# Optimization experiments

Measured on AMD Instinct MI355X. Metric: run time of the kernel, lower is better.

The kernel has to match this reference:

```python
import jax, jax.numpy as jnp
import numpy as np

B, S, E, H, MLP = 2, 2048, 1024, 16, 4096
VEC = 8          # args.vec_length: block-row height of vector-sparse mask
SPARSITY = 0.9   # fraction of attention entries dropped
D = E // H


def _make_mask():
    # static_random_mask_aligned: each block-row of VEC query rows keeps a
    # random ~(1-sparsity) subset of key columns. Diagonal kept so every
    # softmax row is non-empty.
    rng = np.random.default_rng(0)
    block = rng.random((S // VEC, S)) < (1.0 - SPARSITY)   # [m, n]
    mask = np.repeat(block, VEC, axis=0)                   # [S, S]
    mask |= np.eye(S, dtype=bool)
    return jnp.asarray(mask)


def setup_inputs() -> dict:
    key = jax.random.key(0)
    ks = jax.random.split(key, 8)
    w = lambda k, shp: (0.02 * jax.random.normal(k, shp, dtype=jnp.float32))
    return {
        "x": jax.random.normal(ks[0], (B, S, E), dtype=jnp.float32),
        "mask": _make_mask(),                       # [S,S] bool, static
        "w_qkv": w(ks[1], (3 * E, E)),             # in_proj_weight
        "b_qkv": jnp.zeros((3 * E,), jnp.float32),
        "w_out": w(ks[2], (E, E)),                 # out_proj
        "b_out": jnp.zeros((E,), jnp.float32),
        "g1": jnp.ones((E,), jnp.float32), "beta1": jnp.zeros((E,), jnp.float32),
        "g2": jnp.ones((E,), jnp.float32), "beta2": jnp.zeros((E,), jnp.float32),
        "w1": w(ks[3], (MLP, E)), "bias1": jnp.zeros((MLP,), jnp.float32),
        "w2": w(ks[4], (E, MLP)), "bias2": jnp.zeros((E,), jnp.float32),
    }


def _layer_norm(x, g, b, eps=1e-5):
    mu = jnp.mean(x, axis=-1, keepdims=True)
    var = jnp.mean(jnp.square(x - mu), axis=-1, keepdims=True)
    return (x - mu) * jax.lax.rsqrt(var + eps) * g + b


def _sparse_mha(h, mask, w_qkv, b_qkv, w_out, b_out):
    qkv = jnp.einsum("bse,fe->bsf", h, w_qkv) + b_qkv       # [B,S,3E]
    q, k, v = jnp.split(qkv, 3, axis=-1)
    q = q.reshape(B, S, H, D)
    k = k.reshape(B, S, H, D)
    v = v.reshape(B, S, H, D)
    scores = jnp.einsum("bqhd,bkhd->bhqk", q, k) / jnp.sqrt(jnp.float32(D))
    scores = jnp.where(mask[None, None], scores, jnp.float32(-1e9))
    p = jax.nn.softmax(scores, axis=-1)
    ctx = jnp.einsum("bhqk,bkhd->bqhd", p, v).reshape(B, S, E)
    return jnp.einsum("bse,fe->bsf", ctx, w_out) + b_out


def reference(x, mask, w_qkv, b_qkv, w_out, b_out, g1, beta1, g2, beta2,
              w1, bias1, w2, bias2):
    h = _layer_norm(x, g1, beta1)
    attn = _sparse_mha(h, mask, w_qkv, b_qkv, w_out, b_out)
    out = attn + x                      # residual 1
    out = _layer_norm(out, g2, beta2)
    out = jnp.einsum("bse,me->bsm", out, w1) + bias1   # linear1 (no activation, as in source)
    out = jnp.einsum("bsm,em->bse", out, w2) + bias2   # linear2
    return out + x                      # residual adds ORIGINAL x (as in source)
```

## Files before the change

### kernel.cpp

```cpp
#include <hip/hip_runtime.h>
#include <cstdint>
#include <cstddef>

typedef unsigned short u16;
typedef unsigned int u32;
typedef short s16x8 __attribute__((ext_vector_type(8)));
typedef float f32x4 __attribute__((ext_vector_type(4)));
typedef _Float16 f16x2 __attribute__((ext_vector_type(2)));

__device__ __forceinline__ float fdot2(f16x2 a, f16x2 b, float c) {
#if defined(__HIP_DEVICE_COMPILE__) && __has_builtin(__builtin_amdgcn_fdot2)
  return __builtin_amdgcn_fdot2(a, b, c, false);
#else
  return (float)a.x * (float)b.x + (float)a.y * (float)b.y + c;
#endif
}

__device__ __forceinline__ float red8(float x) {
#if defined(__HIP_DEVICE_COMPILE__) && __has_builtin(__builtin_amdgcn_update_dpp)
  int xi = __float_as_int(x);
  x += __int_as_float(__builtin_amdgcn_update_dpp(0, xi, 0xB1, 0xF, 0xF, true));
  xi = __float_as_int(x);
  x += __int_as_float(__builtin_amdgcn_update_dpp(0, xi, 0x4E, 0xF, 0xF, true));
  xi = __float_as_int(x);
  x += __int_as_float(__builtin_amdgcn_update_dpp(0, xi, 0x141, 0xF, 0xF, true));
  return x;
#else
  x += __shfl_xor(x, 1); x += __shfl_xor(x, 2); x += __shfl_xor(x, 4);
  return x;
#endif
}

#define S_LEN 2048
#define EMB   1024
#define NHEAD 16
#define HD    64
#define E3    3072
#define MLPD  4096
#define NROWS 4096
#define LCAP  640

__device__ __forceinline__ float bf2f(u16 v) {
  union { u32 i; float f; } c; c.i = ((u32)v) << 16; return c.f;
}
__device__ __forceinline__ u16 f2bf(float f) {
  union { float f; u32 i; } c; c.f = f;
  u32 x = c.i;
  return (u16)((x + 0x7FFFu + ((x >> 16) & 1u)) >> 16);
}
__device__ __forceinline__ u16 f2h(float f) {
  _Float16 h = (_Float16)f;
  union { _Float16 h; u16 b; } c; c.h = h; return c.b;
}

__device__ __forceinline__ void gl2lds16(const void* g, void* l) {
  __builtin_amdgcn_global_load_lds(
      (__attribute__((address_space(1))) void*)(g),
      (__attribute__((address_space(3))) void*)(l), 16, 0, 0);
}

__global__ void detect_flags(const u32* __restrict__ w1s, int* __restrict__ dtflag,
                             const u32* __restrict__ mask, int* __restrict__ maskrep) {
  __shared__ int hits[256];
  __shared__ u32 red[256];
  int h = 0; u32 v = 0;
  for (int i = threadIdx.x; i < 4096; i += 256) {
    u32 w = w1s[i];
    if ((w & 0xFFFFu) && (((w >> 7) & 0xFFu) >= 0xC8u)) ++h;
    v |= mask[i];
  }
  hits[threadIdx.x] = h; red[threadIdx.x] = v;
  __syncthreads();
  if (threadIdx.x == 0) {
    int t = 0; u32 o = 0;
    for (int i = 0; i < 256; ++i) { t += hits[i]; o |= red[i]; }
    *dtflag = (t > 8) ? 1 : 0;
    int rep;
    if (o <= 1u) rep = 0;
    else if (o & 0x80u) rep = 1;
    else if (o & 0x00800000u) rep = 2;
    else rep = 3;
    *maskrep = rep;
  }
}

__device__ __forceinline__ bool maskbit(const void* m, int rep, size_t idx) {
  switch (rep) {
    case 0:  return ((const int*)m)[idx] != 0;
    case 1:  return ((const u16*)m)[idx] != 0;
    case 2:  return ((const u32*)m)[idx] != 0;
    default: return ((const unsigned char*)m)[idx] != 0;
  }
}

__global__ __launch_bounds__(256)
void cvt_kernel(const void* __restrict__ src, u16* __restrict__ dst,
                int n8, const int* __restrict__ dtflag) {
  const int i = blockIdx.x * blockDim.x + threadIdx.x;
  if (i >= n8) return;
  if (*dtflag) {
    const float4 a = ((const float4*)src)[i * 2];
    const float4 b = ((const float4*)src)[i * 2 + 1];
    u16 o[8] = {f2bf(a.x), f2bf(a.y), f2bf(a.z), f2bf(a.w),
                f2bf(b.x), f2bf(b.y), f2bf(b.z), f2bf(b.w)};
    *(uint4*)(dst + (size_t)i * 8) = *(const uint4*)o;
  } else {
    ((uint4*)dst)[i] = ((const uint4*)src)[i];
  }
}

__global__ void cvt_small(const void* s0, u16* d0, const void* s1, u16* d1,
                          const void* s2, u16* d2, const void* s3, u16* d3,
                          const void* s4, u16* d4, const void* s5, u16* d5,
                          const void* s6, u16* d6, const void* s7, u16* d7,
                          const int* __restrict__ dtflag) {
  const int f = *dtflag;
  const void* srcs[8] = {s0, s1, s2, s3, s4, s5, s6, s7};
  u16* dsts[8] = {d0, d1, d2, d3, d4, d5, d6, d7};
  const int ns[8] = {E3, EMB, EMB, EMB, EMB, EMB, MLPD, EMB};
#pragma unroll
  for (int k = 0; k < 8; ++k) {
    for (int idx = threadIdx.x; idx < ns[k]; idx += 256)
      dsts[k][idx] = f ? f2bf(((const float*)srcs[k])[idx])
                       : ((const u16*)srcs[k])[idx];
  }
}

__global__ void build_lists(const void* __restrict__ mask, const int* __restrict__ repf,
                            int* __restrict__ lists, int* __restrict__ cnt,
                            unsigned char* __restrict__ diagflag) {
  __shared__ int num;
  const int m = blockIdx.x;
  if (threadIdx.x == 0) num = 0;
  __syncthreads();
  const int rep = *repf;
  const int row0 = m * 8;
  for (int j = threadIdx.x; j < S_LEN; j += 256) {
    int srcrow = (j == row0) ? (row0 + 1) : row0;
    bool bit = maskbit(mask, rep, (size_t)srcrow * S_LEN + j);
    if (j >= row0 && j < row0 + 8) diagflag[j] = bit ? 0 : 1;
    if (bit) {
      int p = atomicAdd(&num, 1);
      if (p < LCAP) lists[m * LCAP + p] = j * 2048;
    }
  }
  __syncthreads();
  if (threadIdx.x == 0) cnt[m] = (num < LCAP) ? num : LCAP;
}

__global__ __launch_bounds__(256)
void ln_kernel(const void* __restrict__ Xv, const u16* __restrict__ g,
               const u16* __restrict__ be, u16* __restrict__ O,
               const int* __restrict__ inf32) {
  const int wv = threadIdx.x >> 6, ln = threadIdx.x & 63;
  const int row = blockIdx.x * 4 + wv;
  float v[16];
  if (inf32 && *inf32) {
    const float* xr = (const float*)Xv + (size_t)row * EMB;
    float4 a0 = *(const float4*)(xr + ln * 8);
    float4 a1 = *(const float4*)(xr + ln * 8 + 4);
    float4 b0 = *(const float4*)(xr + 512 + ln * 8);
    float4 b1 = *(const float4*)(xr + 512 + ln * 8 + 4);
    v[0]=a0.x; v[1]=a0.y; v[2]=a0.z; v[3]=a0.w; v[4]=a1.x; v[5]=a1.y; v[6]=a1.z; v[7]=a1.w;
    v[8]=b0.x; v[9]=b0.y; v[10]=b0.z; v[11]=b0.w; v[12]=b1.x; v[13]=b1.y; v[14]=b1.z; v[15]=b1.w;
  } else {
    const u16* xr = (const u16*)Xv + (size_t)row * EMB;
    union { uint4 u; u16 s[8]; } p0, p1;
    p0.u = *(const uint4*)(xr + ln * 8);
    p1.u = *(const uint4*)(xr + 512 + ln * 8);
#pragma unroll
    for (int t = 0; t < 8; ++t) { v[t] = bf2f(p0.s[t]); v[8 + t] = bf2f(p1.s[t]); }
  }
  float s = 0.f, sq = 0.f;
#pragma unroll
  for (int t = 0; t < 16; ++t) { s += v[t]; sq += v[t] * v[t]; }
#pragma unroll
  for (int off = 32; off; off >>= 1) { s += __shfl_xor(s, off); sq += __shfl_xor(sq, off); }
  const float mu = s * (1.0f / EMB);
  const float var = sq * (1.0f / EMB) - mu * mu;
  const float rsig = rsqrtf(var + 1e-5f);
  union { uint4 u; u16 s[8]; } g0, g1v, b0, b1v, o0, o1;
  g0.u = *(const uint4*)(g + ln * 8);   g1v.u = *(const uint4*)(g + 512 + ln * 8);
  b0.u = *(const uint4*)(be + ln * 8);  b1v.u = *(const uint4*)(be + 512 + ln * 8);
#pragma unroll
  for (int t = 0; t < 8; ++t) {
    o0.s[t] = f2bf((v[t]     - mu) * rsig * bf2f(g0.s[t])  + bf2f(b0.s[t]));
    o1.s[t] = f2bf((v[8 + t] - mu) * rsig * bf2f(g1v.s[t]) + bf2f(b1v.s[t]));
  }
  u16* orow = O + (size_t)row * EMB;
  *(uint4*)(orow + ln * 8) = o0.u;
  *(uint4*)(orow + 512 + ln * 8) = o1.u;
}

__global__ __launch_bounds__(256)
void gemm_bt(const u16* __restrict__ A, const u16* __restrict__ B,
             const u16* __restrict__ bias, u16* __restrict__ C,
             int M, int N, int K) {
  __shared__ u16 a_sh[128 * 64];
  __shared__ u16 b_sh[128 * 64];
  const int tid = threadIdx.x;
  const int wv = tid >> 6, ln = tid & 63;
  const int wm = wv & 1, wn = wv >> 1;
  const int tm = blockIdx.y, tn = blockIdx.x;
  const int srow = ln >> 3;
  const int scol = ((ln & 7) ^ srow) * 8;
  const int q = ln >> 4, rr = ln & 15;

  f32x4 acc[4][4] = {};
  const u16* Abase = A + (size_t)(tm * 128) * K;
  const u16* Bbase = B + (size_t)(tn * 128) * K;

  for (int k0 = 0; k0 < K; k0 += 64) {
    __syncthreads();
#pragma unroll
    for (int c = 0; c < 4; ++c) {
      const int chunk = wv * 4 + c;
      const int row = chunk * 8 + srow;
      gl2lds16(Abase + (size_t)row * K + k0 + scol, &a_sh[chunk * 512]);
      gl2lds16(Bbase + (size_t)row * K + k0 + scol, &b_sh[chunk * 512]);
    }
    __syncthreads();
#pragma unroll
    for (int kk = 0; kk < 2; ++kk) {
      const int slot = ((kk * 4 + q) ^ (rr & 7)) * 8;
      s16x8 af[4], bfr[4];
#pragma unroll
      for (int mi = 0; mi < 4; ++mi)
        af[mi] = *(const s16x8*)&a_sh[(wm * 64 + mi * 16 + rr) * 64 + slot];
#pragma unroll
      for (int ni = 0; ni < 4; ++ni)
        bfr[ni] = *(const s16x8*)&b_sh[(wn * 64 + ni * 16 + rr) * 64 + slot];
#pragma unroll
      for (int mi = 0; mi < 4; ++mi)
#pragma unroll
        for (int ni = 0; ni < 4; ++ni)
          acc[mi][ni] = __builtin_amdgcn_mfma_f32_16x16x32_bf16(af[mi], bfr[ni], acc[mi][ni], 0, 0, 0);
    }
  }
#pragma unroll
  for (int ni = 0; ni < 4; ++ni) {
    const int col = tn * 128 + wn * 64 + ni * 16 + rr;
    const float bv = bf2f(bias[col]);
#pragma unroll
    for (int mi = 0; mi < 4; ++mi)
#pragma unroll
      for (int r2 = 0; r2 < 4; ++r2) {
        const int row = tm * 128 + wm * 64 + mi * 16 + q * 4 + r2;
        C[(size_t)row * N + col] = f2bf(acc[mi][ni][r2] + bv);
      }
  }
}

__global__ __launch_bounds__(256)
void gemm_bt_sk(const u16* __restrict__ A, const u16* __restrict__ B,
                u16* __restrict__ P0, u16* __restrict__ P1,
                int M, int N, int K) {
  __shared__ u16 a_sh[128 * 64];
  __shared__ u16 b_sh[128 * 64];
  const int tid = threadIdx.x;
  const int wv = tid >> 6, ln = tid & 63;
  const int wm = wv & 1, wn = wv >> 1;
  const int tm = blockIdx.y, tn = blockIdx.x, kz = blockIdx.z;
  const int Kh = K >> 1;
  const int koff = kz * Kh;
  const int srow = ln >> 3;
  const int scol = ((ln & 7) ^ srow) * 8;
  const int q = ln >> 4, rr = ln & 15;

  f32x4 acc[4][4] = {};
  const u16* Abase = A + (size_t)(tm * 128) * K + koff;
  const u16* Bbase = B + (size_t)(tn * 128) * K + koff;

  for (int k0 = 0; k0 < Kh; k0 += 64) {
    __syncthreads();
#pragma unroll
    for (int c = 0; c < 4; ++c) {
      const int chunk = wv * 4 + c;
      const int row = chunk * 8 + srow;
      gl2lds16(Abase + (size_t)row * K + k0 + scol, &a_sh[chunk * 512]);
      gl2lds16(Bbase + (size_t)row * K + k0 + scol, &b_sh[chunk * 512]);
    }
    __syncthreads();
#pragma unroll
    for (int kk = 0; kk < 2; ++kk) {
      const int slot = ((kk * 4 + q) ^ (rr & 7)) * 8;
      s16x8 af[4], bfr[4];
#pragma unroll
      for (int mi = 0; mi < 4; ++mi)
        af[mi] = *(const s16x8*)&a_sh[(wm * 64 + mi * 16 + rr) * 64 + slot];
#pragma unroll
      for (int ni = 0; ni < 4; ++ni)
        bfr[ni] = *(const s16x8*)&b_sh[(wn * 64 + ni * 16 + rr) * 64 + slot];
#pragma unroll
      for (int mi = 0; mi < 4; ++mi)
#pragma unroll
        for (int ni = 0; ni < 4; ++ni)
          acc[mi][ni] = __builtin_amdgcn_mfma_f32_16x16x32_bf16(af[mi], bfr[ni], acc[mi][ni], 0, 0, 0);
    }
  }
  u16* P = kz ? P1 : P0;
#pragma unroll
  for (int ni = 0; ni < 4; ++ni) {
    const int col = tn * 128 + wn * 64 + ni * 16 + rr;
#pragma unroll
    for (int mi = 0; mi < 4; ++mi)
#pragma unroll
      for (int r2 = 0; r2 < 4; ++r2) {
        const int row = tm * 128 + wm * 64 + mi * 16 + q * 4 + r2;
        P[(size_t)row * N + col] = f2bf(acc[mi][ni][r2]);
      }
  }
}

__global__ __launch_bounds__(256)
void combine_kernel(const u16* __restrict__ P0, const u16* __restrict__ P1,
                    const u16* __restrict__ bias, const void* __restrict__ xr,
                    void* __restrict__ Ov, const int* __restrict__ f32io) {
  const int i = blockIdx.x * 256 + threadIdx.x;
  const int col8 = (i & 127) * 8;
  union { uint4 u; u16 s[8]; } a, b, bi;
  a.u = ((const uint4*)P0)[i];
  b.u = ((const uint4*)P1)[i];
  bi.u = *(const uint4*)(bias + col8);
  const int f = *f32io;
  float o[8];
#pragma unroll
  for (int t = 0; t < 8; ++t) o[t] = bf2f(a.s[t]) + bf2f(b.s[t]) + bf2f(bi.s[t]);
  if (f) {
    const float4 x0 = ((const float4*)xr)[i * 2];
    const float4 x1 = ((const float4*)xr)[i * 2 + 1];
    o[0]+=x0.x; o[1]+=x0.y; o[2]+=x0.z; o[3]+=x0.w;
    o[4]+=x1.x; o[5]+=x1.y; o[6]+=x1.z; o[7]+=x1.w;
    float4 r0 = {o[0],o[1],o[2],o[3]}, r1 = {o[4],o[5],o[6],o[7]};
    ((float4*)Ov)[i * 2] = r0;
    ((float4*)Ov)[i * 2 + 1] = r1;
  } else {
    union { uint4 u; u16 s[8]; } xv;
    xv.u = ((const uint4*)xr)[i];
    u16 r[8];
#pragma unroll
    for (int t = 0; t < 8; ++t) r[t] = f2bf(o[t] + bf2f(xv.s[t]));
    ((uint4*)Ov)[i] = *(const uint4*)r;
  }
}

__global__ __launch_bounds__(256)
void gemm_qkv(const u16* __restrict__ A, const u16* __restrict__ B,
              const u16* __restrict__ bias,
              u16* __restrict__ Qb, u16* __restrict__ Kp, u16* __restrict__ Vp,
              int K) {
  __shared__ u16 a_sh[128 * 64];
  __shared__ u16 b_sh[128 * 64];
  const int tid = threadIdx.x;
  const int wv = tid >> 6, ln = tid & 63;
  const int wm = wv & 1, wn = wv >> 1;
  const int tm = blockIdx.y, tn = blockIdx.x;
  const int srow = ln >> 3;
  const int scol = ((ln & 7) ^ srow) * 8;
  const int q = ln >> 4, rr = ln & 15;

  f32x4 acc[4][4] = {};
  const u16* Abase = A + (size_t)(tm * 128) * K;
  const u16* Bbase = B + (size_t)(tn * 128) * K;

  for (int k0 = 0; k0 < K; k0 += 64) {
    __syncthreads();
#pragma unroll
    for (int c = 0; c < 4; ++c) {
      const int chunk = wv * 4 + c;
      const int row = chunk * 8 + srow;
      gl2lds16(Abase + (size_t)row * K + k0 + scol, &a_sh[chunk * 512]);
      gl2lds16(Bbase + (size_t)row * K + k0 + scol, &b_sh[chunk * 512]);
    }
    __syncthreads();
#pragma unroll
    for (int kk = 0; kk < 2; ++kk) {
      const int slot = ((kk * 4 + q) ^ (rr & 7)) * 8;
      s16x8 af[4], bfr[4];
#pragma unroll
      for (int mi = 0; mi < 4; ++mi)
        af[mi] = *(const s16x8*)&a_sh[(wm * 64 + mi * 16 + rr) * 64 + slot];
#pragma unroll
      for (int ni = 0; ni < 4; ++ni)
        bfr[ni] = *(const s16x8*)&b_sh[(wn * 64 + ni * 16 + rr) * 64 + slot];
#pragma unroll
      for (int mi = 0; mi < 4; ++mi)
#pragma unroll
        for (int ni = 0; ni < 4; ++ni)
          acc[mi][ni] = __builtin_amdgcn_mfma_f32_16x16x32_bf16(af[mi], bfr[ni], acc[mi][ni], 0, 0, 0);
    }
  }
  const int third = (tn * 128) >> 10;
#pragma unroll
  for (int ni = 0; ni < 4; ++ni) {
    const int col = tn * 128 + wn * 64 + ni * 16 + rr;
    const int w = col & 1023;
    const float bv = bf2f(bias[col]);
#pragma unroll
    for (int mi = 0; mi < 4; ++mi)
#pragma unroll
      for (int r2 = 0; r2 < 4; ++r2) {
        const int row = tm * 128 + wm * 64 + mi * 16 + q * 4 + r2;
        const float o = acc[mi][ni][r2] + bv;
        const size_t idx = (size_t)row * 1024 + w;
        if (third == 0)      Qb[idx] = f2bf(o);
        else if (third == 1) Kp[idx] = f2h(o);
        else                 Vp[idx] = f2h(o);
      }
  }
}

__global__ __launch_bounds__(256)
void gemm_bt_n64(const u16* __restrict__ A, const u16* __restrict__ B,
                 const u16* __restrict__ bias, const void* __restrict__ resid,
                 void* __restrict__ Cv, int M, int N, int K,
                 const int* __restrict__ residf32, const int* __restrict__ outf32) {
  __shared__ u16 a_sh[128 * 64];
  __shared__ u16 b_sh[64 * 64];
  const int tid = threadIdx.x;
  const int wv = tid >> 6, ln = tid & 63;
  const int wm = wv & 1, wn = wv >> 1;
  const int tm = blockIdx.y, tn = blockIdx.x;
  const int srow = ln >> 3;
  const int scol = ((ln & 7) ^ srow) * 8;
  const int q = ln >> 4, rr = ln & 15;

  f32x4 acc[4][2] = {};
  const u16* Abase = A + (size_t)(tm * 128) * K;
  const u16* Bbase = B + (size_t)(tn * 64) * K;

  for (int k0 = 0; k0 < K; k0 += 64) {
    __syncthreads();
#pragma unroll
    for (int c = 0; c < 4; ++c) {
      const int chunk = wv * 4 + c;
      const int row = chunk * 8 + srow;
      gl2lds16(Abase + (size_t)row * K + k0 + scol, &a_sh[chunk * 512]);
    }
#pragma unroll
    for (int c = 0; c < 2; ++c) {
      const int chunk = wv * 2 + c;
      const int row = chunk * 8 + srow;
      gl2lds16(Bbase + (size_t)row * K + k0 + scol, &b_sh[chunk * 512]);
    }
    __syncthreads();
#pragma unroll
    for (int kk = 0; kk < 2; ++kk) {
      const int slot = ((kk * 4 + q) ^ (rr & 7)) * 8;
      s16x8 af[4], bfr[2];
#pragma unroll
      for (int mi = 0; mi < 4; ++mi)
        af[mi] = *(const s16x8*)&a_sh[(wm * 64 + mi * 16 + rr) * 64 + slot];
#pragma unroll
      for (int ni = 0; ni < 2; ++ni)
        bfr[ni] = *(const s16x8*)&b_sh[(wn * 32 + ni * 16 + rr) * 64 + slot];
#pragma unroll
      for (int mi = 0; mi < 4; ++mi)
#pragma unroll
        for (int ni = 0; ni < 2; ++ni)
          acc[mi][ni] = __builtin_amdgcn_mfma_f32_16x16x32_bf16(af[mi], bfr[ni], acc[mi][ni], 0, 0, 0);
    }
  }
  const int rf32 = residf32 ? *residf32 : 0;
  const int f32o = outf32 ? *outf32 : 0;
#pragma unroll
  for (int ni = 0; ni < 2; ++ni) {
    const int col = tn * 64 + wn * 32 + ni * 16 + rr;
    const float bv = bf2f(bias[col]);
#pragma unroll
    for (int mi = 0; mi < 4; ++mi)
#pragma unroll
      for (int r2 = 0; r2 < 4; ++r2) {
        const int row = tm * 128 + wm * 64 + mi * 16 + q * 4 + r2;
        const size_t idx = (size_t)row * N + col;
        float o = acc[mi][ni][r2] + bv;
        if (resid)
          o += rf32 ? ((const float*)resid)[idx] : bf2f(((const u16*)resid)[idx]);
        if (f32o) ((float*)Cv)[idx] = o;
        else      ((u16*)Cv)[idx] = f2bf(o);
      }
  }
}

__global__ __launch_bounds__(512)
void attn_kernel(const u16* __restrict__ Qb, const u16* __restrict__ Kp,
                 const u16* __restrict__ Vp, const int* __restrict__ lists,
                 const int* __restrict__ cnt, const unsigned char* __restrict__ diagflag,
                 u16* __restrict__ ctx) {
  __shared__ int list_sh[LCAP];
  const int g = blockIdx.x;
  const int b = g >> 12;
  const int h = (g >> 8) & 15;
  const int m = g & 255;
  const int tid = threadIdx.x, wv = tid >> 6, ln = tid & 63;
  const int es = ln >> 3, dc = ln & 7;
  const int i = m * 8 + wv;
  const int n = cnt[m];

  for (int e = tid; e < n; e += 512) list_sh[e] = lists[m * LCAP + e];
  __syncthreads();

  const u16* qrow = Qb + (size_t)(b * S_LEN + i) * EMB + h * 64 + dc * 8;
  union { uint4 u; u16 s[8]; } qi; qi.u = *(const uint4*)qrow;
  f16x2 q2[4];
#pragma unroll
  for (int t = 0; t < 4; ++t) {
    q2[t].x = (_Float16)(bf2f(qi.s[2 * t])     * 0.125f);
    q2[t].y = (_Float16)(bf2f(qi.s[2 * t + 1]) * 0.125f);
  }

  const char* kbase = (const char*)Kp + (size_t)b * S_LEN * 2048 + h * 128 + dc * 16;
  const char* vbase = (const char*)Vp + (size_t)b * S_LEN * 2048 + h * 128 + dc * 16;

  float sum = 0.f;
  float acc[8] = {};

  auto score = [&](const uint4& ku) -> float {
    union { uint4 u; f16x2 p[4]; } kk; kk.u = ku;
    float s = fdot2(kk.p[3], q2[3], fdot2(kk.p[2], q2[2],
              fdot2(kk.p[1], q2[1], fdot2(kk.p[0], q2[0], 0.f))));
    s = red8(s);
    return __expf(fminf(fmaxf(s, -60.f), 60.f));
  };
  auto doV = [&](const uint4& vu, float p) {
    union { uint4 u; _Float16 hh[8]; } vv; vv.u = vu;
#pragma unroll
    for (int t = 0; t < 8; ++t) acc[t] += (float)vv.hh[t] * p;
  };

  const int df = diagflag[i];
  if (df) {
    const int dioff = i * 2048;
    const uint4 ku = *(const uint4*)(kbase + dioff);
    const uint4 vu = *(const uint4*)(vbase + dioff);
    float p = score(ku);
    p = (es == 0) ? p : 0.f;
    sum += p;
    doV(vu, p);
  }

  int e0 = 0;
  for (; e0 + 32 <= n; e0 += 32) {
    const int oA = list_sh[e0 + es];
    const int oB = list_sh[e0 + 8 + es];
    const int oC = list_sh[e0 + 16 + es];
    const int oD = list_sh[e0 + 24 + es];
    const uint4 kA = *(const uint4*)(kbase + (size_t)oA);
    const uint4 kB = *(const uint4*)(kbase + (size_t)oB);
    const uint4 kC = *(const uint4*)(kbase + (size_t)oC);
    const uint4 kD = *(const uint4*)(kbase + (size_t)oD);
    const uint4 vA = *(const uint4*)(vbase + (size_t)oA);
    const uint4 vB = *(const uint4*)(vbase + (size_t)oB);
    const uint4 vC = *(const uint4*)(vbase + (size_t)oC);
    const uint4 vD = *(const uint4*)(vbase + (size_t)oD);
    const float pA = score(kA);
    const float pB = score(kB);
    const float pC = score(kC);
    const float pD = score(kD);
    sum += (pA + pB) + (pC + pD);
    doV(vA, pA);
    doV(vB, pB);
    doV(vC, pC);
    doV(vD, pD);
  }
  for (; e0 + 8 <= n; e0 += 8) {
    const int off = list_sh[e0 + es];
    const uint4 ku = *(const uint4*)(kbase + (size_t)off);
    const uint4 vu = *(const uint4*)(vbase + (size_t)off);
    const float p = score(ku);
    sum += p;
    doV(vu, p);
  }
  if (e0 < n) {
    const int e = e0 + es;
    const bool valid = (e < n);
    const int off = valid ? list_sh[e] : list_sh[0];
    const uint4 ku = *(const uint4*)(kbase + (size_t)off);
    const uint4 vu = *(const uint4*)(vbase + (size_t)off);
    float p = score(ku);
    p = valid ? p : 0.f;
    sum += p;
    doV(vu, p);
  }

#pragma unroll
  for (int off = 8; off < 64; off <<= 1) {
    sum += __shfl_xor(sum, off);
#pragma unroll
    for (int t = 0; t < 8; ++t) acc[t] += __shfl_xor(acc[t], off);
  }

  if (es == 0) {
    const float inv = 1.0f / sum;
    u16 o[8];
#pragma unroll
    for (int t = 0; t < 8; ++t) o[t] = f2bf(acc[t] * inv);
    *(uint4*)(ctx + (size_t)(b * S_LEN + i) * EMB + h * 64 + dc * 8) = *(const uint4*)o;
  }
}

extern "C" void kernel_launch(void* const* d_in, const int* in_sizes, int n_in,
                              void* d_out, int out_size, void* d_ws, size_t ws_size,
                              hipStream_t stream) {
  const void* x_raw    = d_in[0];
  const void* mask     = d_in[1];
  const void* wqkv_raw = d_in[2];
  const void* bqkv_raw = d_in[3];
  const void* wout_raw = d_in[4];
  const void* bout_raw = d_in[5];
  const void* g1_raw   = d_in[6];
  const void* be1_raw  = d_in[7];
  const void* g2_raw   = d_in[8];
  const void* be2_raw  = d_in[9];
  const void* w1_raw   = d_in[10];
  const void* b1_raw   = d_in[11];
  const void* w2_raw   = d_in[12];
  const void* b2_raw   = d_in[13];

  char* ws = (char*)d_ws;
  const size_t MB = 1u << 20;
  int* dtflag         = (int*)ws;
  int* maskrep        = (int*)(ws + 64);
  int* cnt            = (int*)(ws + 1024);
  unsigned char* dfl  = (unsigned char*)(ws + 4096);
  int* lists          = (int*)(ws + 8192);
  u16* R1  = (u16*)(ws + 1 * MB);
  u16* Qb  = (u16*)(ws + 9 * MB);
  u16* Kp  = (u16*)(ws + 17 * MB);
  u16* Vp  = (u16*)(ws + 25 * MB);
  u16* M1  = (u16*)(ws + 17 * MB);
  u16* W   = (u16*)(ws + 49 * MB);
  char* sm = ws + 57 * MB;
  u16* bq  = (u16*)(sm);
  u16* bo  = (u16*)(sm + 8192);
  u16* g1b = (u16*)(sm + 16384);
  u16* be1b= (u16*)(sm + 24576);
  u16* g2b = (u16*)(sm + 32768);
  u16* be2b= (u16*)(sm + 40960);
  u16* b1b = (u16*)(sm + 49152);
  u16* b2b = (u16*)(sm + 65536);

  detect_flags<<<dim3(1), dim3(256), 0, stream>>>((const u32*)w1_raw, dtflag,
                                                  (const u32*)mask, maskrep);
  build_lists<<<dim3(256), dim3(256), 0, stream>>>(mask, maskrep, lists, cnt, dfl);
  cvt_small<<<dim3(1), dim3(256), 0, stream>>>(
      bqkv_raw, bq, bout_raw, bo, g1_raw, g1b, be1_raw, be1b,
      g2_raw, g2b, be2_raw, be2b, b1_raw, b1b, b2_raw, b2b, dtflag);

  auto cvt = [&](const void* src, u16* dst, int n) {
    const int n8 = n / 8;
    cvt_kernel<<<dim3((n8 + 255) / 256), dim3(256), 0, stream>>>(src, dst, n8, dtflag);
  };

  ln_kernel<<<dim3(NROWS / 4), dim3(256), 0, stream>>>(x_raw, g1b, be1b, R1, dtflag);
  cvt(wqkv_raw, W, E3 * EMB);
  gemm_qkv<<<dim3(E3 / 128, NROWS / 128), dim3(256), 0, stream>>>(
      R1, W, bq, Qb, Kp, Vp, EMB);
  attn_kernel<<<dim3(2 * NHEAD * 256), dim3(512), 0, stream>>>(
      Qb, Kp, Vp, lists, cnt, dfl, R1);
  cvt(wout_raw, W, EMB * EMB);
  gemm_bt_n64<<<dim3(EMB / 64, NROWS / 128), dim3(256), 0, stream>>>(
      R1, W, bo, x_raw, Qb, NROWS, EMB, EMB, dtflag, nullptr);
  ln_kernel<<<dim3(NROWS / 4), dim3(256), 0, stream>>>(Qb, g2b, be2b, R1, nullptr);
  cvt(w1_raw, W, MLPD * EMB);
  gemm_bt<<<dim3(MLPD / 128, NROWS / 128), dim3(256), 0, stream>>>(
      R1, W, b1b, M1, NROWS, MLPD, EMB);
  cvt(w2_raw, W, EMB * MLPD);
  gemm_bt_sk<<<dim3(EMB / 128, NROWS / 128, 2), dim3(256), 0, stream>>>(
      M1, W, R1, Qb, NROWS, EMB, MLPD);
  combine_kernel<<<dim3(NROWS * EMB / 8 / 256), dim3(256), 0, stream>>>(
      R1, Qb, b2b, x_raw, d_out, dtflag);
}
```

Measured before the change: 456.9 us.

## Interleave K and V per head and use fma_mix/exp2 in sparse attention

The QKV GEMM now writes K and V into one interleaved buffer where each head's K and V rows sit side by side, so each gathered key's K and V loads hit adjacent 128-byte segments, with 32-bit offsets instead of size_t. The attention inner loop folds log2(e) into the query scale and uses exp2f, replaces the fp16-to-fp32 convert-and-FMA in the V accumulation with v_fma_mix_f32 inline asm, and writes the DPP reduction as inline v_add_f32_dpp. These aim to cut memory transactions and VALU instructions in the gather-bound attention loop. The exp clamp range changes and inline asm brings portability and correctness risk.

```diff
diff --git a/kernel.cpp b/kernel.cpp
--- a/kernel.cpp
+++ b/kernel.cpp
@@ -17,17 +17,34 @@
 }
 
 __device__ __forceinline__ float red8(float x) {
-#if defined(__HIP_DEVICE_COMPILE__) && __has_builtin(__builtin_amdgcn_update_dpp)
-  int xi = __float_as_int(x);
-  x += __int_as_float(__builtin_amdgcn_update_dpp(0, xi, 0xB1, 0xF, 0xF, true));
-  xi = __float_as_int(x);
-  x += __int_as_float(__builtin_amdgcn_update_dpp(0, xi, 0x4E, 0xF, 0xF, true));
-  xi = __float_as_int(x);
-  x += __int_as_float(__builtin_amdgcn_update_dpp(0, xi, 0x141, 0xF, 0xF, true));
+#if defined(__HIP_DEVICE_COMPILE__)
+  asm("v_add_f32_dpp %0, %0, %0 quad_perm:[1,0,3,2] row_mask:0xf bank_mask:0xf"
+      : "+v"(x));
+  asm("v_add_f32_dpp %0, %0, %0 quad_perm:[2,3,0,1] row_mask:0xf bank_mask:0xf"
+      : "+v"(x));
+  asm("v_add_f32_dpp %0, %0, %0 row_half_mirror row_mask:0xf bank_mask:0xf"
+      : "+v"(x));
   return x;
 #else
   x += __shfl_xor(x, 1); x += __shfl_xor(x, 2); x += __shfl_xor(x, 4);
   return x;
+#endif
+}
+
+__device__ __forceinline__ void fmamix_lo(float& a, u32 hv, float p) {
+#if defined(__HIP_DEVICE_COMPILE__)
+  asm("v_fma_mix_f32 %0, %1, %2, %0 op_sel_hi:[1,0,0]"
+      : "+v"(a) : "v"(hv), "v"(p));
+#else
+  union { u32 i; _Float16 h[2]; } c; c.i = hv; a += (float)c.h[0] * p;
+#endif
+}
+__device__ __forceinline__ void fmamix_hi(float& a, u32 hv, float p) {
+#if defined(__HIP_DEVICE_COMPILE__)
+  asm("v_fma_mix_f32 %0, %1, %2, %0 op_sel:[1,0,0] op_sel_hi:[1,0,0]"
+      : "+v"(a) : "v"(hv), "v"(p));
+#else
+  union { u32 i; _Float16 h[2]; } c; c.i = hv; a += (float)c.h[1] * p;
 #endif
 }
 
@@ -141,7 +158,7 @@
     if (j >= row0 && j < row0 + 8) diagflag[j] = bit ? 0 : 1;
     if (bit) {
       int p = atomicAdd(&num, 1);
-      if (p < LCAP) lists[m * LCAP + p] = j * 2048;
+      if (p < LCAP) lists[m * LCAP + p] = j * 4096;
     }
   }
   __syncthreads();
@@ -347,7 +364,7 @@
 __global__ __launch_bounds__(256)
 void gemm_qkv(const u16* __restrict__ A, const u16* __restrict__ B,
               const u16* __restrict__ bias,
-              u16* __restrict__ Qb, u16* __restrict__ Kp, u16* __restrict__ Vp,
+              u16* __restrict__ Qb, u16* __restrict__ KVp,
               int K) {
   __shared__ u16 a_sh[128 * 64];
   __shared__ u16 b_sh[128 * 64];
@@ -402,10 +419,12 @@
       for (int r2 = 0; r2 < 4; ++r2) {
         const int row = tm * 128 + wm * 64 + mi * 16 + q * 4 + r2;
         const float o = acc[mi][ni][r2] + bv;
-        const size_t idx = (size_t)row * 1024 + w;
-        if (third == 0)      Qb[idx] = f2bf(o);
-        else if (third == 1) Kp[idx] = f2h(o);
-        else                 Vp[idx] = f2h(o);
+        if (third == 0) {
+          Qb[(size_t)row * 1024 + w] = f2bf(o);
+        } else {
+          const int hh = w >> 6, d = w & 63;
+          KVp[(size_t)row * 2048 + hh * 128 + ((third == 1) ? 0 : 64) + d] = f2h(o);
+        }
       }
   }
 }
@@ -483,8 +502,8 @@
 }
 
 __global__ __launch_bounds__(512)
-void attn_kernel(const u16* __restrict__ Qb, const u16* __restrict__ Kp,
-                 const u16* __restrict__ Vp, const int* __restrict__ lists,
+void attn_kernel(const u16* __restrict__ Qb, const u16* __restrict__ KVp,
+                 const int* __restrict__ lists,
                  const int* __restrict__ cnt, const unsigned char* __restrict__ diagflag,
                  u16* __restrict__ ctx) {
   __shared__ int list_sh[LCAP];
@@ -503,14 +522,15 @@
   const u16* qrow = Qb + (size_t)(b * S_LEN + i) * EMB + h * 64 + dc * 8;
   union { uint4 u; u16 s[8]; } qi; qi.u = *(const uint4*)qrow;
   f16x2 q2[4];
+  const float qs = 0.125f * 1.44269504f;
 #pragma unroll
   for (int t = 0; t < 4; ++t) {
-    q2[t].x = (_Float16)(bf2f(qi.s[2 * t])     * 0.125f);
-    q2[t].y = (_Float16)(bf2f(qi.s[2 * t + 1]) * 0.125f);
-  }
-
-  const char* kbase = (const char*)Kp + (size_t)b * S_LEN * 2048 + h * 128 + dc * 16;
-  const char* vbase = (const char*)Vp + (size_t)b * S_LEN * 2048 + h * 128 + dc * 16;
+    q2[t].x = (_Float16)(bf2f(qi.s[2 * t])     * qs);
+    q2[t].y = (_Float16)(bf2f(qi.s[2 * t + 1]) * qs);
+  }
+
+  const char* kvb = (const char*)KVp + (size_t)b * S_LEN * 4096;
+  const u32 loff = (u32)(h * 256 + dc * 16);
 
   float sum = 0.f;
   float acc[8] = {};
@@ -520,19 +540,21 @@
     float s = fdot2(kk.p[3], q2[3], fdot2(kk.p[2], q2[2],
               fdot2(kk.p[1], q2[1], fdot2(kk.p[0], q2[0], 0.f))));
     s = red8(s);
-    return __expf(fminf(fmaxf(s, -60.f), 60.f));
+    s = fminf(fmaxf(s, -126.f), 126.f);
+    return exp2f(s);
   };
   auto doV = [&](const uint4& vu, float p) {
-    union { uint4 u; _Float16 hh[8]; } vv; vv.u = vu;
-#pragma unroll
-    for (int t = 0; t < 8; ++t) acc[t] += (float)vv.hh[t] * p;
+    fmamix_lo(acc[0], vu.x, p); fmamix_hi(acc[1], vu.x, p);
+    fmamix_lo(acc[2], vu.y, p); fmamix_hi(acc[3], vu.y, p);
+    fmamix_lo(acc[4], vu.z, p); fmamix_hi(acc[5], vu.z, p);
+    fmamix_lo(acc[6], vu.w, p); fmamix_hi(acc[7], vu.w, p);
   };
 
   const int df = diagflag[i];
   if (df) {
-    const int dioff = i * 2048;
-    const uint4 ku = *(const uint4*)(kbase + dioff);
-    const uint4 vu = *(const uint4*)(vbase + dioff);
+    const u32 dioff = (u32)(i * 4096) + loff;
+    const uint4 ku = *(const uint4*)(kvb + dioff);
+    const uint4 vu = *(const uint4*)(kvb + dioff + 128);
     float p = score(ku);
     p = (es == 0) ? p : 0.f;
     sum += p;
@@ -541,18 +563,18 @@
 
   int e0 = 0;
   for (; e0 + 32 <= n; e0 += 32) {
-    const int oA = list_sh[e0 + es];
-    const int oB = list_sh[e0 + 8 + es];
-    const int oC = list_sh[e0 + 16 + es];
-    const int oD = list_sh[e0 + 24 + es];
-    const uint4 kA = *(const uint4*)(kbase + (size_t)oA);
-    const uint4 kB = *(const uint4*)(kbase + (size_t)oB);
-    const uint4 kC = *(const uint4*)(kbase + (size_t)oC);
-    const uint4 kD = *(const uint4*)(kbase + (size_t)oD);
-    const uint4 vA = *(const uint4*)(vbase + (size_t)oA);
-    const uint4 vB = *(const uint4*)(vbase + (size_t)oB);
-    const uint4 vC = *(const uint4*)(vbase + (size_t)oC);
-    const uint4 vD = *(const uint4*)(vbase + (size_t)oD);
+    const u32 oA = (u32)list_sh[e0 + es] + loff;
+    const u32 oB = (u32)list_sh[e0 + 8 + es] + loff;
+    const u32 oC = (u32)list_sh[e0 + 16 + es] + loff;
+    const u32 oD = (u32)list_sh[e0 + 24 + es] + loff;
+    const uint4 kA = *(const uint4*)(kvb + oA);
+    const uint4 kB = *(const uint4*)(kvb + oB);
+    const uint4 kC = *(const uint4*)(kvb + oC);
+    const uint4 kD = *(const uint4*)(kvb + oD);
+    const uint4 vA = *(const uint4*)(kvb + oA + 128);
+    const uint4 vB = *(const uint4*)(kvb + oB + 128);
+    const uint4 vC = *(const uint4*)(kvb + oC + 128);
+    const uint4 vD = *(const uint4*)(kvb + oD + 128);
     const float pA = score(kA);
     const float pB = score(kB);
     const float pC = score(kC);
@@ -564,9 +586,9 @@
     doV(vD, pD);
   }
   for (; e0 + 8 <= n; e0 += 8) {
-    const int off = list_sh[e0 + es];
-    const uint4 ku = *(const uint4*)(kbase + (size_t)off);
-    const uint4 vu = *(const uint4*)(vbase + (size_t)off);
+    const u32 off = (u32)list_sh[e0 + es] + loff;
+    const uint4 ku = *(const uint4*)(kvb + off);
+    const uint4 vu = *(const uint4*)(kvb + off + 128);
     const float p = score(ku);
     sum += p;
     doV(vu, p);
@@ -574,9 +596,9 @@
   if (e0 < n) {
     const int e = e0 + es;
     const bool valid = (e < n);
-    const int off = valid ? list_sh[e] : list_sh[0];
-    const uint4 ku = *(const uint4*)(kbase + (size_t)off);
-    const uint4 vu = *(const uint4*)(vbase + (size_t)off);
+    const u32 off = (u32)(valid ? list_sh[e] : list_sh[0]) + loff;
+    const uint4 ku = *(const uint4*)(kvb + off);
+    const uint4 vu = *(const uint4*)(kvb + off + 128);
     float p = score(ku);
     p = valid ? p : 0.f;
     sum += p;
@@ -626,8 +648,7 @@
   int* lists          = (int*)(ws + 8192);
   u16* R1  = (u16*)(ws + 1 * MB);
   u16* Qb  = (u16*)(ws + 9 * MB);
-  u16* Kp  = (u16*)(ws + 17 * MB);
-  u16* Vp  = (u16*)(ws + 25 * MB);
+  u16* KVp = (u16*)(ws + 17 * MB);
   u16* M1  = (u16*)(ws + 17 * MB);
   u16* W   = (u16*)(ws + 49 * MB);
   char* sm = ws + 57 * MB;
@@ -655,9 +676,9 @@
   ln_kernel<<<dim3(NROWS / 4), dim3(256), 0, stream>>>(x_raw, g1b, be1b, R1, dtflag);
   cvt(wqkv_raw, W, E3 * EMB);
   gemm_qkv<<<dim3(E3 / 128, NROWS / 128), dim3(256), 0, stream>>>(
-      R1, W, bq, Qb, Kp, Vp, EMB);
+      R1, W, bq, Qb, KVp, EMB);
   attn_kernel<<<dim3(2 * NHEAD * 256), dim3(512), 0, stream>>>(
-      Qb, Kp, Vp, lists, cnt, dfl, R1);
+      Qb, KVp, lists, cnt, dfl, R1);
   cvt(wout_raw, W, EMB * EMB);
   gemm_bt_n64<<<dim3(EMB / 64, NROWS / 128), dim3(256), 0, stream>>>(
       R1, W, bo, x_raw, Qb, NROWS, EMB, EMB, dtflag, nullptr);
```

Measured after the change: 469.2 us. 2.7% more time.

## Rewrite sparse attention with MFMA over interleaved per-head KV layout

Applied to the files above, without the earlier changes.

Attention is restructured so that each wave handles one 8-row query block and computes QK^T and PV with f16 MFMA instructions over 16-key chunks, replacing the scalar fdot2/DPP-reduction path. The QKV GEMM epilogue now writes K and V interleaved per (batch, head) in 256-byte rows, and pre-scales Q by 1/sqrt(d)*log2(e) in fp16 so exp2 can be used. The aim is to move score and context math onto matrix cores and to fetch K and V from one contiguous row. In exchange it adds an LDS transpose of V per chunk and fp16 probabilities, and it drops the max-subtraction in favour of a clamp.

```diff
diff --git a/kernel.cpp b/kernel.cpp
--- a/kernel.cpp
+++ b/kernel.cpp
@@ -4,32 +4,11 @@
 
 typedef unsigned short u16;
 typedef unsigned int u32;
+typedef unsigned long long u64;
 typedef short s16x8 __attribute__((ext_vector_type(8)));
 typedef float f32x4 __attribute__((ext_vector_type(4)));
-typedef _Float16 f16x2 __attribute__((ext_vector_type(2)));
-
-__device__ __forceinline__ float fdot2(f16x2 a, f16x2 b, float c) {
-#if defined(__HIP_DEVICE_COMPILE__) && __has_builtin(__builtin_amdgcn_fdot2)
-  return __builtin_amdgcn_fdot2(a, b, c, false);
-#else
-  return (float)a.x * (float)b.x + (float)a.y * (float)b.y + c;
-#endif
-}
-
-__device__ __forceinline__ float red8(float x) {
-#if defined(__HIP_DEVICE_COMPILE__) && __has_builtin(__builtin_amdgcn_update_dpp)
-  int xi = __float_as_int(x);
-  x += __int_as_float(__builtin_amdgcn_update_dpp(0, xi, 0xB1, 0xF, 0xF, true));
-  xi = __float_as_int(x);
-  x += __int_as_float(__builtin_amdgcn_update_dpp(0, xi, 0x4E, 0xF, 0xF, true));
-  xi = __float_as_int(x);
-  x += __int_as_float(__builtin_amdgcn_update_dpp(0, xi, 0x141, 0xF, 0xF, true));
-  return x;
-#else
-  x += __shfl_xor(x, 1); x += __shfl_xor(x, 2); x += __shfl_xor(x, 4);
-  return x;
-#endif
-}
+typedef _Float16 f16x4 __attribute__((ext_vector_type(4)));
+typedef _Float16 f16x8 __attribute__((ext_vector_type(8)));
 
 #define S_LEN 2048
 #define EMB   1024
@@ -141,7 +120,7 @@
     if (j >= row0 && j < row0 + 8) diagflag[j] = bit ? 0 : 1;
     if (bit) {
       int p = atomicAdd(&num, 1);
-      if (p < LCAP) lists[m * LCAP + p] = j * 2048;
+      if (p < LCAP) lists[m * LCAP + p] = j * 256;
     }
   }
   __syncthreads();
@@ -347,7 +326,7 @@
 __global__ __launch_bounds__(256)
 void gemm_qkv(const u16* __restrict__ A, const u16* __restrict__ B,
               const u16* __restrict__ bias,
-              u16* __restrict__ Qb, u16* __restrict__ Kp, u16* __restrict__ Vp,
+              u16* __restrict__ Qb, u16* __restrict__ KVp,
               int K) {
   __shared__ u16 a_sh[128 * 64];
   __shared__ u16 b_sh[128 * 64];
@@ -391,6 +370,7 @@
     }
   }
   const int third = (tn * 128) >> 10;
+  const float QS = 0.125f * 1.44269504f;
 #pragma unroll
   for (int ni = 0; ni < 4; ++ni) {
     const int col = tn * 128 + wn * 64 + ni * 16 + rr;
@@ -402,10 +382,14 @@
       for (int r2 = 0; r2 < 4; ++r2) {
         const int row = tm * 128 + wm * 64 + mi * 16 + q * 4 + r2;
         const float o = acc[mi][ni][r2] + bv;
-        const size_t idx = (size_t)row * 1024 + w;
-        if (third == 0)      Qb[idx] = f2bf(o);
-        else if (third == 1) Kp[idx] = f2h(o);
-        else                 Vp[idx] = f2h(o);
+        if (third == 0) {
+          Qb[(size_t)row * 1024 + w] = f2h(o * QS);
+        } else {
+          const int hh = w >> 6, d = w & 63;
+          const int bq_ = row >> 11, s = row & 2047;
+          KVp[((size_t)(bq_ * NHEAD + hh) * S_LEN + s) * 128 +
+              ((third == 1) ? 0 : 64) + d] = f2h(o);
+        }
       }
   }
 }
@@ -482,120 +466,122 @@
   }
 }
 
-__global__ __launch_bounds__(512)
-void attn_kernel(const u16* __restrict__ Qb, const u16* __restrict__ Kp,
-                 const u16* __restrict__ Vp, const int* __restrict__ lists,
+__global__ __launch_bounds__(256)
+void attn_kernel(const u16* __restrict__ Qb, const u16* __restrict__ KVp,
+                 const int* __restrict__ lists,
                  const int* __restrict__ cnt, const unsigned char* __restrict__ diagflag,
                  u16* __restrict__ ctx) {
-  __shared__ int list_sh[LCAP];
+  __shared__ int list_sh[4][LCAP];
+  __shared__ uint4 vsh4[4][128];
   const int g = blockIdx.x;
-  const int b = g >> 12;
-  const int h = (g >> 8) & 15;
-  const int m = g & 255;
+  const int bh = g & 31;
+  const int mq = g >> 5;
+  const int b = bh >> 4, h = bh & 15;
   const int tid = threadIdx.x, wv = tid >> 6, ln = tid & 63;
-  const int es = ln >> 3, dc = ln & 7;
-  const int i = m * 8 + wv;
+  const int lg = ln >> 4;
+  const int dl = ln & 15;
+  const int m = mq * 4 + wv;
+  const int i0 = m * 8;
+
+#pragma unroll
+  for (int w = 0; w < 4; ++w) {
+    const int nw = cnt[mq * 4 + w];
+    for (int e = tid; e < nw; e += 256) list_sh[w][e] = lists[(mq * 4 + w) * LCAP + e];
+  }
+  __syncthreads();
+
   const int n = cnt[m];
-
-  for (int e = tid; e < n; e += 512) list_sh[e] = lists[m * LCAP + e];
-  __syncthreads();
-
-  const u16* qrow = Qb + (size_t)(b * S_LEN + i) * EMB + h * 64 + dc * 8;
-  union { uint4 u; u16 s[8]; } qi; qi.u = *(const uint4*)qrow;
-  f16x2 q2[4];
-#pragma unroll
-  for (int t = 0; t < 4; ++t) {
-    q2[t].x = (_Float16)(bf2f(qi.s[2 * t])     * 0.125f);
-    q2[t].y = (_Float16)(bf2f(qi.s[2 * t + 1]) * 0.125f);
-  }
-
-  const char* kbase = (const char*)Kp + (size_t)b * S_LEN * 2048 + h * 128 + dc * 16;
-  const char* vbase = (const char*)Vp + (size_t)b * S_LEN * 2048 + h * 128 + dc * 16;
-
-  float sum = 0.f;
-  float acc[8] = {};
-
-  auto score = [&](const uint4& ku) -> float {
-    union { uint4 u; f16x2 p[4]; } kk; kk.u = ku;
-    float s = fdot2(kk.p[3], q2[3], fdot2(kk.p[2], q2[2],
-              fdot2(kk.p[1], q2[1], fdot2(kk.p[0], q2[0], 0.f))));
-    s = red8(s);
-    return __expf(fminf(fmaxf(s, -60.f), 60.f));
+  const u64 du = *(const u64*)(diagflag + i0);
+
+  f16x8 qb0 = {}, qb1 = {};
+  if (dl < 8) {
+    const u16* qr = Qb + (size_t)(b * S_LEN + i0 + dl) * EMB + h * 64 + lg * 8;
+    union { uint4 u; f16x8 h; } a0, a1;
+    a0.u = *(const uint4*)qr;
+    a1.u = *(const uint4*)(qr + 32);
+    qb0 = a0.h; qb1 = a1.h;
+  }
+
+  const char* kvb = (const char*)KVp + (size_t)bh * S_LEN * 256;
+
+  uint4* vwp = &vsh4[wv][0];
+  const int widx = ((lg >> 1) << 5) + ((dl & 3) << 3) + ((dl >> 2) << 1) + (lg & 1);
+  const u16* vrp = (const u16*)vwp + (lg << 4) + dl;
+
+  float rs = 0.f;
+  f32x4 acc[4] = {};
+
+  auto CHUNK = [&](int c0, int mode) {
+    int le;
+    if (mode == 2) {
+      le = (i0 + (dl & 7)) * 256;
+    } else {
+      const int e = c0 + dl;
+      const int idx = (mode == 1 && e >= n) ? 0 : e;
+      le = list_sh[wv][idx];
+    }
+    const char* base = kvb + le + (lg << 4);
+    union { uint4 u; f16x8 h; } ka0, ka1;
+    ka0.u = *(const uint4*)(base);
+    ka1.u = *(const uint4*)(base + 64);
+    const uint4 v0 = *(const uint4*)(base + 128);
+    const uint4 v1 = *(const uint4*)(base + 192);
+
+    f32x4 st = {};
+    st = __builtin_amdgcn_mfma_f32_16x16x32_f16(ka0.h, qb0, st, 0, 0, 0);
+    st = __builtin_amdgcn_mfma_f32_16x16x32_f16(ka1.h, qb1, st, 0, 0, 0);
+
+    vwp[widx] = v0;
+    vwp[widx + 64] = v1;
+
+    _Float16 ph[4];
+#pragma unroll
+    for (int r = 0; r < 4; ++r) {
+      float s = st[r];
+      s = fminf(fmaxf(s, -126.f), 15.f);
+      float p = exp2f(s);
+      bool keep = true;
+      const int e2 = (lg << 2) + r;
+      if (mode == 1) keep = (c0 + e2) < n;
+      if (mode == 2) keep = (e2 == dl) && (((du >> ((e2 & 7) * 8)) & 1ull) != 0ull);
+      p = keep ? p : 0.f;
+      ph[r] = (_Float16)p;
+      rs += (float)ph[r];
+    }
+    const f16x4 pa = { ph[0], ph[1], ph[2], ph[3] };
+
+#pragma unroll
+    for (int dc = 0; dc < 4; ++dc) {
+      union { u16 s[4]; f16x4 h; } bf;
+      bf.s[0] = vrp[dc * 256 +   0];
+      bf.s[1] = vrp[dc * 256 +  64];
+      bf.s[2] = vrp[dc * 256 + 128];
+      bf.s[3] = vrp[dc * 256 + 192];
+      acc[dc] = __builtin_amdgcn_mfma_f32_16x16x16f16(pa, bf.h, acc[dc], 0, 0, 0);
+    }
   };
-  auto doV = [&](const uint4& vu, float p) {
-    union { uint4 u; _Float16 hh[8]; } vv; vv.u = vu;
-#pragma unroll
-    for (int t = 0; t < 8; ++t) acc[t] += (float)vv.hh[t] * p;
-  };
-
-  const int df = diagflag[i];
-  if (df) {
-    const int dioff = i * 2048;
-    const uint4 ku = *(const uint4*)(kbase + dioff);
-    const uint4 vu = *(const uint4*)(vbase + dioff);
-    float p = score(ku);
-    p = (es == 0) ? p : 0.f;
-    sum += p;
-    doV(vu, p);
-  }
-
-  int e0 = 0;
-  for (; e0 + 32 <= n; e0 += 32) {
-    const int oA = list_sh[e0 + es];
-    const int oB = list_sh[e0 + 8 + es];
-    const int oC = list_sh[e0 + 16 + es];
-    const int oD = list_sh[e0 + 24 + es];
-    const uint4 kA = *(const uint4*)(kbase + (size_t)oA);
-    const uint4 kB = *(const uint4*)(kbase + (size_t)oB);
-    const uint4 kC = *(const uint4*)(kbase + (size_t)oC);
-    const uint4 kD = *(const uint4*)(kbase + (size_t)oD);
-    const uint4 vA = *(const uint4*)(vbase + (size_t)oA);
-    const uint4 vB = *(const uint4*)(vbase + (size_t)oB);
-    const uint4 vC = *(const uint4*)(vbase + (size_t)oC);
-    const uint4 vD = *(const uint4*)(vbase + (size_t)oD);
-    const float pA = score(kA);
-    const float pB = score(kB);
-    const float pC = score(kC);
-    const float pD = score(kD);
-    sum += (pA + pB) + (pC + pD);
-    doV(vA, pA);
-    doV(vB, pB);
-    doV(vC, pC);
-    doV(vD, pD);
-  }
-  for (; e0 + 8 <= n; e0 += 8) {
-    const int off = list_sh[e0 + es];
-    const uint4 ku = *(const uint4*)(kbase + (size_t)off);
-    const uint4 vu = *(const uint4*)(vbase + (size_t)off);
-    const float p = score(ku);
-    sum += p;
-    doV(vu, p);
-  }
-  if (e0 < n) {
-    const int e = e0 + es;
-    const bool valid = (e < n);
-    const int off = valid ? list_sh[e] : list_sh[0];
-    const uint4 ku = *(const uint4*)(kbase + (size_t)off);
-    const uint4 vu = *(const uint4*)(vbase + (size_t)off);
-    float p = score(ku);
-    p = valid ? p : 0.f;
-    sum += p;
-    doV(vu, p);
-  }
-
-#pragma unroll
-  for (int off = 8; off < 64; off <<= 1) {
-    sum += __shfl_xor(sum, off);
-#pragma unroll
-    for (int t = 0; t < 8; ++t) acc[t] += __shfl_xor(acc[t], off);
-  }
-
-  if (es == 0) {
-    const float inv = 1.0f / sum;
-    u16 o[8];
-#pragma unroll
-    for (int t = 0; t < 8; ++t) o[t] = f2bf(acc[t] * inv);
-    *(uint4*)(ctx + (size_t)(b * S_LEN + i) * EMB + h * 64 + dc * 8) = *(const uint4*)o;
+
+  int c0 = 0;
+  for (; c0 + 16 <= n; c0 += 16) CHUNK(c0, 0);
+  if (c0 < n) CHUNK(c0, 1);
+  CHUNK(0, 2);
+
+  rs += __shfl_xor(rs, 16);
+  rs += __shfl_xor(rs, 32);
+
+  float invs[4];
+#pragma unroll
+  for (int r = 0; r < 4; ++r) invs[r] = __shfl(rs, (lg << 2) + r);
+
+  if (lg < 2) {
+#pragma unroll
+    for (int r = 0; r < 4; ++r) {
+      const float inv = 1.0f / invs[r];
+      u16* orow = ctx + (size_t)(b * S_LEN + i0 + (lg << 2) + r) * EMB + h * 64 + dl;
+#pragma unroll
+      for (int dc = 0; dc < 4; ++dc)
+        orow[dc * 16] = f2bf(acc[dc][r] * inv);
+    }
   }
 }
 
@@ -626,8 +612,7 @@
   int* lists          = (int*)(ws + 8192);
   u16* R1  = (u16*)(ws + 1 * MB);
   u16* Qb  = (u16*)(ws + 9 * MB);
-  u16* Kp  = (u16*)(ws + 17 * MB);
-  u16* Vp  = (u16*)(ws + 25 * MB);
+  u16* KVp = (u16*)(ws + 17 * MB);
   u16* M1  = (u16*)(ws + 17 * MB);
   u16* W   = (u16*)(ws + 49 * MB);
   char* sm = ws + 57 * MB;
@@ -655,9 +640,9 @@
   ln_kernel<<<dim3(NROWS / 4), dim3(256), 0, stream>>>(x_raw, g1b, be1b, R1, dtflag);
   cvt(wqkv_raw, W, E3 * EMB);
   gemm_qkv<<<dim3(E3 / 128, NROWS / 128), dim3(256), 0, stream>>>(
-      R1, W, bq, Qb, Kp, Vp, EMB);
-  attn_kernel<<<dim3(2 * NHEAD * 256), dim3(512), 0, stream>>>(
-      Qb, Kp, Vp, lists, cnt, dfl, R1);
+      R1, W, bq, Qb, KVp, EMB);
+  attn_kernel<<<dim3(2 * NHEAD * 64), dim3(256), 0, stream>>>(
+      Qb, KVp, lists, cnt, dfl, R1);
   cvt(wout_raw, W, EMB * EMB);
   gemm_bt_n64<<<dim3(EMB / 64, NROWS / 128), dim3(256), 0, stream>>>(
       R1, W, bo, x_raw, Qb, NROWS, EMB, EMB, dtflag, nullptr);
```

After: 411.6 us. -9.9%, faster.
